# Kernel tuning notes

Measured on AMD Instinct MI355X. Metric: run time of the kernel, lower is better.

Reference implementation:

```python
import jax, jax.numpy as jnp
import numpy as np

N, E, NB = 50000, 100000, 6          # nodes, directed messages, max neighbors
NF, BF, H, DEPTH = 98, 6, 256, 6     # node feat, bond feat, hidden, depth
EF = NF + BF                          # edge_fdim: hmess = [fnode[src], bond_feats]


def setup_inputs() -> dict:
    key = jax.random.key(0)
    ks = jax.random.split(key, 12)
    s = lambda fan: np.float32(1.0 / np.sqrt(fan))
    return {
        "fnode": jax.random.normal(ks[0], (N, NF), jnp.float32),
        "fmess_idx": jax.random.randint(ks[1], (E, 2), 0, N),
        "fmess_feat": jax.random.normal(ks[2], (E, BF), jnp.float32),
        "agraph": jax.random.randint(ks[3], (N, NB), 0, E),
        "bgraph": jax.random.randint(ks[4], (E, NB), 0, E),
        "Wz": jax.random.normal(ks[5], (3, EF + H, H), jnp.float32) * s(EF + H),
        "bz": jnp.zeros((3, H), jnp.float32),
        "Wr": jax.random.normal(ks[6], (3, EF, H), jnp.float32) * s(EF),
        "Ur": jax.random.normal(ks[7], (3, H, H), jnp.float32) * s(H),
        "bur": jnp.zeros((3, H), jnp.float32),
        "Wh": jax.random.normal(ks[8], (3, EF + H, H), jnp.float32) * s(EF + H),
        "bh": jnp.zeros((3, H), jnp.float32),
        "Wo": jax.random.normal(ks[9], (3, NF + H, H), jnp.float32) * s(NF + H),
        "bo": jnp.zeros((3, H), jnp.float32),
    }


def _mpn(hnode, hmess, agraph, bgraph, Wz, bz, Wr, Ur, bur, Wh, bh, Wo, bo):
    # One MPNLayer: depth-unrolled message GRU over bgraph, then node readout via agraph.
    e_mask = jnp.ones((hmess.shape[0], 1), hmess.dtype).at[0, 0].set(0.0)  # msg 0 = padding
    r1 = hmess @ Wr  # W_r(fmess), loop-invariant  [E,H]

    def step(h, _):
        h_nei = h[bgraph]                                    # [E,NB,H] gather inbound msgs
        sum_h = h_nei.sum(axis=1)
        z = jax.nn.sigmoid(jnp.concatenate([hmess, sum_h], axis=1) @ Wz + bz)
        r = jax.nn.sigmoid(r1[:, None, :] + h_nei @ Ur + bur)  # [E,NB,H]
        sum_gh = (r * h_nei).sum(axis=1)
        pre_h = jnp.tanh(jnp.concatenate([hmess, sum_gh], axis=1) @ Wh + bh)
        return ((1.0 - z) * sum_h + z * pre_h) * e_mask, None

    h0 = jnp.zeros((hmess.shape[0], bz.shape[0]), hmess.dtype)
    h, _ = jax.lax.scan(step, h0, None, length=DEPTH)
    nei = h[agraph].sum(axis=1)                              # [N,H]
    node_h = jax.nn.relu(jnp.concatenate([hnode, nei], axis=1) @ Wo + bo)
    n_mask = jnp.ones((hnode.shape[0], 1), hnode.dtype).at[0, 0].set(0.0)  # node 0 = padding
    return node_h * n_mask


def reference(fnode, fmess_idx, fmess_feat, agraph, bgraph,
              Wz, bz, Wr, Ur, bur, Wh, bh, Wo, bo):
    # embed_graph: gather source-node features, concat with bond features
    hmess = jnp.concatenate([fnode[fmess_idx[:, 0]], fmess_feat], axis=1)  # [E,EF]
    run = jax.vmap(lambda a, b, c, d, e, f, g, hh, i: _mpn(
        fnode, hmess, agraph, bgraph, a, b, c, d, e, f, g, hh, i))
    qkv = run(Wz, bz, Wr, Ur, bur, Wh, bh, Wo, bo)           # [3,N,H]: Q/K/V encoders batched
    return (qkv[0], qkv[1], qkv[2])
```

## Files before the change

### kernel.cpp

```cpp
#include <hip/hip_runtime.h>


#define NE 100000
#define NEP 100032
#define NN 50000

typedef unsigned short u16;
typedef short short8 __attribute__((ext_vector_type(8)));
typedef float f32x4 __attribute__((ext_vector_type(4)));
typedef unsigned short u16x4 __attribute__((ext_vector_type(4)));

__device__ __forceinline__ float b2f(u16 u) {
  union { unsigned int i; float f; } v; v.i = ((unsigned int)u) << 16; return v.f;
}
__device__ __forceinline__ u16 f2b(float f) {
  union { float f; unsigned int i; } v; v.f = f;
  unsigned int b = v.i;
  b += 0x7FFFu + ((b >> 16) & 1u);
  return (u16)(b >> 16);
}
__device__ __forceinline__ unsigned cvtpk(float lo, float hi) {
  unsigned r;
  asm("v_cvt_pk_bf16_f32 %0, %1, %2" : "=v"(r) : "v"(lo), "v"(hi));
  return r;
}
__device__ __forceinline__ float sigm(float x) { return 1.0f / (1.0f + __expf(-x)); }
__device__ __forceinline__ float tanh_f(float x) { return 2.0f / (1.0f + __expf(-2.0f * x)) - 1.0f; }
__device__ __forceinline__ f32x4 mfma16(short8 a, short8 b, f32x4 c) {
  return __builtin_amdgcn_mfma_f32_16x16x32_bf16(a, b, c, 0, 0, 0);
}

__global__ void pack_wpre(const float* __restrict__ Wr, const float* __restrict__ Wz,
                          const float* __restrict__ Wh, u16* __restrict__ dst) {
  const int g = blockIdx.y;
  const int p = blockIdx.x * 256 + threadIdx.x;
  const int j = p & 7, l = (p >> 3) & 63, q = p >> 9;
  const int nb = q % 48, s = q / 48;
  const int k = 32 * s + 8 * (l >> 4) + j;
  const int n = 16 * nb + (l & 15);
  float v = 0.f;
  if (k < 104) {
    if (n < 256)      v = Wr[((size_t)g * 104 + k) * 256 + n];
    else if (n < 512) v = Wz[((size_t)g * 360 + k) * 256 + (n - 256)];
    else              v = Wh[((size_t)g * 360 + k) * 256 + (n - 512)];
  }
  dst[(size_t)g * 98304 + p] = f2b(v);
}

__global__ void pack_wgate(const float* __restrict__ Wz, const float* __restrict__ Wh,
                           u16* __restrict__ dst) {
  const int g = blockIdx.y;
  const int p = blockIdx.x * 256 + threadIdx.x;
  const int j = p & 7, l = (p >> 3) & 63, q = p >> 9;
  const int nb = q % 32, s = q / 32;
  const int k = 32 * s + 8 * (l >> 4) + j;
  const int n = 16 * nb + (l & 15);
  float v = (n < 256) ? Wz[((size_t)g * 360 + 104 + k) * 256 + n]
                      : Wh[((size_t)g * 360 + 104 + k) * 256 + (n - 256)];
  dst[(size_t)g * 131072 + p] = f2b(v);
}

__global__ void pack_ur(const float* __restrict__ Ur, u16* __restrict__ dst) {
  const int g = blockIdx.y;
  const int p = blockIdx.x * 256 + threadIdx.x;
  const int j = p & 7, l = (p >> 3) & 63, q = p >> 9;
  const int nb = q % 16, s = q / 16;
  const int k = 32 * s + 8 * (l >> 4) + j;
  const int n = 16 * nb + (l & 15);
  dst[(size_t)g * 65536 + p] = f2b(Ur[((size_t)g * 256 + k) * 256 + n]);
}

__global__ void pack_wo(const float* __restrict__ Wo, u16* __restrict__ dst) {
  const int g = blockIdx.y;
  const int p = blockIdx.x * 256 + threadIdx.x;
  const int j = p & 7, l = (p >> 3) & 63, q = p >> 9;
  const int nb = q % 16, s = q / 16;
  const int k = 32 * s + 8 * (l >> 4) + j;
  const int n = 16 * nb + (l & 15);
  float v = 0.f;
  if (k < 98)        v = Wo[((size_t)g * 354 + k) * 256 + n];
  else if (k >= 128) v = Wo[((size_t)g * 354 + (k - 30)) * 256 + n];
  dst[(size_t)g * 98304 + p] = f2b(v);
}

__global__ void embed_hmess_f(const float* __restrict__ fnode, const int* __restrict__ fmess_idx,
                              const float* __restrict__ fmess_feat, u16* __restrict__ hmF) {
  const int e = blockIdx.x * 2 + (threadIdx.x >> 7);
  const int c = threadIdx.x & 127;
  const int src = fmess_idx[e * 2];
  float v = 0.f;
  if (c < 98)       v = fnode[(size_t)src * 98 + c];
  else if (c < 104) v = fmess_feat[(size_t)e * 6 + (c - 98)];
  hmF[(size_t)(e >> 4) * 2048 + ((c >> 5) * 64 + (e & 15) + 16 * ((c >> 3) & 3)) * 8 + (c & 7)] = f2b(v);
}

__global__ void embed_fnode(const float* __restrict__ fnode, u16* __restrict__ fnp) {
  const int n = blockIdx.x * 2 + (threadIdx.x >> 7);
  const int c = threadIdx.x & 127;
  float v = (c < 98) ? fnode[(size_t)n * 98 + c] : 0.f;
  fnp[(size_t)n * 128 + c] = f2b(v);
}

__global__ __launch_bounds__(256)
void pre_gemm_t(const u16* __restrict__ hmF, const u16* __restrict__ Wpre,
                const float* __restrict__ bur, const float* __restrict__ bz,
                const float* __restrict__ bh, u16* __restrict__ r1b,
                u16* __restrict__ zpF, u16* __restrict__ hpF) {
  const int tid = threadIdx.x, wave = tid >> 6, lane = tid & 63;
  const int row0 = lane & 15, kq = lane >> 4;
  const int e0 = blockIdx.x * 32;
  const int cchunk = blockIdx.y;
  f32x4 acc[2][4];
#pragma unroll
  for (int i = 0; i < 2; ++i)
#pragma unroll
    for (int n = 0; n < 4; ++n) { acc[i][n][0]=0.f; acc[i][n][1]=0.f; acc[i][n][2]=0.f; acc[i][n][3]=0.f; }
#pragma unroll
  for (int kc = 0; kc < 4; ++kc) {
    short8 bf[2];
#pragma unroll
    for (int ef = 0; ef < 2; ++ef)
      bf[ef] = *(const short8*)(hmF + (size_t)((e0 >> 4) + ef) * 2048 + (size_t)(kc * 64 + lane) * 8);
#pragma unroll
    for (int nf = 0; nf < 4; ++nf) {
      const int nb = cchunk * 16 + wave * 4 + nf;
      short8 wf = *(const short8*)(Wpre + ((size_t)(kc * 48 + nb) * 64 + lane) * 8);
      acc[0][nf] = mfma16(wf, bf[0], acc[0][nf]);
      acc[1][nf] = mfma16(wf, bf[1], acc[1][nf]);
    }
  }
  const float* bias = (cchunk == 0) ? bur : (cchunk == 1 ? bz : bh);
  u16* dstF = (cchunk == 1) ? zpF : hpF;
#pragma unroll
  for (int ef = 0; ef < 2; ++ef)
#pragma unroll
    for (int nf = 0; nf < 4; ++nf) {
      const int n256 = wave * 64 + nf * 16 + kq * 4;
      const int e = e0 + ef * 16 + row0;
      u16x4 o;
#pragma unroll
      for (int v = 0; v < 4; ++v) o[v] = f2b(acc[ef][nf][v] + bias[n256 + v]);
      if (cchunk == 0) {
        *(u16x4*)(r1b + (size_t)e * 256 + n256) = o;
      } else {
        *(u16x4*)(dstF + ((size_t)((e0 >> 4) + ef) * 16 + (wave * 4 + nf)) * 256 + lane * 4) = o;
      }
    }
}

__global__ __launch_bounds__(512, 4)
void mpn_fused(const u16* __restrict__ HBin, u16* __restrict__ HBout,
               const u16* __restrict__ r1b, const int* __restrict__ bgraph,
               const u16* __restrict__ zpF, const u16* __restrict__ hpF,
               const u16* __restrict__ Wgate, const u16* __restrict__ Urp) {
  __shared__ __align__(16) u16 sF[16384];
  const int tid = threadIdx.x;
  const int wn = tid >> 6, lane = tid & 63;
  const int row0 = lane & 15, kq = lane >> 4;
  const int e0 = blockIdx.x * 32;

  {
    const int c0 = 4 * lane;
    const int offc = ((c0 >> 5) * 64 + 16 * ((c0 >> 3) & 3)) * 8 + (c0 & 7);
#pragma unroll 2
    for (int rr = 0; rr < 4; ++rr) {
      const int r = wn * 4 + rr;
      const int e = e0 + r;
      const u16x4 r1v = *(const u16x4*)(r1b + (size_t)e * 256 + c0);
      int idx[6];
#pragma unroll
      for (int k = 0; k < 6; ++k) idx[k] = bgraph[e * 6 + k];
      u16x4 hv[6], huv[6];
#pragma unroll
      for (int k = 0; k < 6; ++k) {
        const u16* rowp = HBin + (size_t)idx[k] * 512;
        hv[k]  = *(const u16x4*)(rowp + c0);
        huv[k] = *(const u16x4*)(rowp + 256 + c0);
      }
      float sh[4] = {0.f, 0.f, 0.f, 0.f}, sg[4] = {0.f, 0.f, 0.f, 0.f};
#pragma unroll
      for (int k = 0; k < 6; ++k)
#pragma unroll
        for (int j = 0; j < 4; ++j) {
          const float h  = b2f(hv[k][j]);
          const float rg = sigm(b2f(r1v[j]) + b2f(huv[k][j]));
          sh[j] += h;
          sg[j] += rg * h;
        }
      const int off = (r >> 4) * 4096 + offc + (r & 15) * 8;
      union { unsigned w[2]; u16x4 q; } p0, p1;
      p0.w[0] = cvtpk(sh[0], sh[1]); p0.w[1] = cvtpk(sh[2], sh[3]);
      p1.w[0] = cvtpk(sg[0], sg[1]); p1.w[1] = cvtpk(sg[2], sg[3]);
      *(u16x4*)(sF + off) = p0.q;
      *(u16x4*)(sF + 8192 + off) = p1.q;
    }
  }
  __syncthreads();

  f32x4 aZ[2][2], aH[2][2];
#pragma unroll
  for (int nf = 0; nf < 2; ++nf)
#pragma unroll
    for (int ef = 0; ef < 2; ++ef) {
      aZ[nf][ef][0]=0.f; aZ[nf][ef][1]=0.f; aZ[nf][ef][2]=0.f; aZ[nf][ef][3]=0.f;
      aH[nf][ef][0]=0.f; aH[nf][ef][1]=0.f; aH[nf][ef][2]=0.f; aH[nf][ef][3]=0.f;
    }
#pragma unroll
  for (int kc = 0; kc < 8; ++kc) {
    short8 wz0 = *(const short8*)(Wgate + ((size_t)(kc * 32 + wn * 2 + 0) * 64 + lane) * 8);
    short8 wz1 = *(const short8*)(Wgate + ((size_t)(kc * 32 + wn * 2 + 1) * 64 + lane) * 8);
    short8 wh0 = *(const short8*)(Wgate + ((size_t)(kc * 32 + 16 + wn * 2 + 0) * 64 + lane) * 8);
    short8 wh1 = *(const short8*)(Wgate + ((size_t)(kc * 32 + 16 + wn * 2 + 1) * 64 + lane) * 8);
#pragma unroll
    for (int ef = 0; ef < 2; ++ef) {
      short8 bsh = *(const short8*)(sF + ef * 4096 + (kc * 64 + lane) * 8);
      short8 bsg = *(const short8*)(sF + 8192 + ef * 4096 + (kc * 64 + lane) * 8);
      aZ[0][ef] = mfma16(wz0, bsh, aZ[0][ef]);
      aZ[1][ef] = mfma16(wz1, bsh, aZ[1][ef]);
      aH[0][ef] = mfma16(wh0, bsg, aH[0][ef]);
      aH[1][ef] = mfma16(wh1, bsg, aH[1][ef]);
    }
  }

  u16x4 hq[2][2];
#pragma unroll
  for (int nf = 0; nf < 2; ++nf) {
    const int lp = row0 + 16 * (nf * 2 + (kq >> 1));
    const int jo = 4 * (kq & 1);
    const int nc = wn * 2 + nf;
#pragma unroll
    for (int ef = 0; ef < 2; ++ef) {
      const int e = e0 + ef * 16 + row0;
      const int as = ef * 4096 + (wn * 64 + lp) * 8 + jo;
      const u16x4 shv = *(const u16x4*)(sF + as);
      const size_t tb = ((size_t)((e0 >> 4) + ef) * 16 + nc) * 256 + lane * 4;
      const u16x4 zp4 = *(const u16x4*)(zpF + tb);
      const u16x4 hp4 = *(const u16x4*)(hpF + tb);
      float hf[4];
#pragma unroll
      for (int v = 0; v < 4; ++v) {
        const float z  = sigm(b2f(zp4[v]) + aZ[nf][ef][v]);
        const float ph = tanh_f(b2f(hp4[v]) + aH[nf][ef][v]);
        float h = (1.0f - z) * b2f(shv[v]) + z * ph;
        if (e == 0) h = 0.f;
        hf[v] = h;
      }
      union { unsigned w[2]; u16x4 q; } pk;
      pk.w[0] = cvtpk(hf[0], hf[1]);
      pk.w[1] = cvtpk(hf[2], hf[3]);
      hq[nf][ef] = pk.q;
    }
  }
  __syncthreads();

#pragma unroll
  for (int nf = 0; nf < 2; ++nf) {
    const int lp = row0 + 16 * (nf * 2 + (kq >> 1));
    const int jo = 4 * (kq & 1);
#pragma unroll
    for (int ef = 0; ef < 2; ++ef)
      *(u16x4*)(sF + 8192 + ef * 4096 + (wn * 64 + lp) * 8 + jo) = hq[nf][ef];
  }
  __syncthreads();

  f32x4 aU[2][2];
#pragma unroll
  for (int nf = 0; nf < 2; ++nf)
#pragma unroll
    for (int ef = 0; ef < 2; ++ef) { aU[nf][ef][0]=0.f; aU[nf][ef][1]=0.f; aU[nf][ef][2]=0.f; aU[nf][ef][3]=0.f; }
#pragma unroll
  for (int kc = 0; kc < 8; ++kc) {
    short8 u0 = *(const short8*)(Urp + ((size_t)(kc * 16 + wn * 2 + 0) * 64 + lane) * 8);
    short8 u1 = *(const short8*)(Urp + ((size_t)(kc * 16 + wn * 2 + 1) * 64 + lane) * 8);
#pragma unroll
    for (int ef = 0; ef < 2; ++ef) {
      short8 hb = *(const short8*)(sF + 8192 + ef * 4096 + (kc * 64 + lane) * 8);
      aU[0][ef] = mfma16(u0, hb, aU[0][ef]);
      aU[1][ef] = mfma16(u1, hb, aU[1][ef]);
    }
  }

  {
    const int r = tid >> 4;
    const int e = e0 + r;
#pragma unroll
    for (int it = 0; it < 2; ++it) {
      const int c = (tid & 15) * 8 + it * 128;
      const short8 val = *(const short8*)(sF + 8192 + (r >> 4) * 4096 +
                         (((c >> 5) * 64 + (r & 15) + 16 * ((c >> 3) & 3)) * 8));
      *(short8*)(HBout + (size_t)e * 512 + c) = val;
    }
  }
#pragma unroll
  for (int nf = 0; nf < 2; ++nf) {
    const int lp = row0 + 16 * (nf * 2 + (kq >> 1));
    const int jo = 4 * (kq & 1);
#pragma unroll
    for (int ef = 0; ef < 2; ++ef) {
      union { unsigned w[2]; u16x4 q; } pk;
      pk.w[0] = cvtpk(aU[nf][ef][0], aU[nf][ef][1]);
      pk.w[1] = cvtpk(aU[nf][ef][2], aU[nf][ef][3]);
      *(u16x4*)(sF + ef * 4096 + (wn * 64 + lp) * 8 + jo) = pk.q;
    }
  }
  __syncthreads();

  {
    const int r = tid >> 4;
    const int e = e0 + r;
#pragma unroll
    for (int it = 0; it < 2; ++it) {
      const int c = (tid & 15) * 8 + it * 128;
      const short8 val = *(const short8*)(sF + (r >> 4) * 4096 +
                         (((c >> 5) * 64 + (r & 15) + 16 * ((c >> 3) & 3)) * 8));
      *(short8*)(HBout + (size_t)e * 512 + 256 + c) = val;
    }
  }
}

__global__ __launch_bounds__(512, 4)
void step0(u16* __restrict__ HB, const u16* __restrict__ zpF, const u16* __restrict__ hpF,
           const u16* __restrict__ Urp) {
  __shared__ __align__(16) u16 sHn[16384];
  const int tid = threadIdx.x;
  const int wn = tid >> 6, lane = tid & 63;
  const int row0 = lane & 15, kq = lane >> 4;
  const int e0 = blockIdx.x * 64;

#pragma unroll
  for (int nf = 0; nf < 2; ++nf) {
    const int lp = row0 + 16 * (nf * 2 + (kq >> 1));
    const int jo = 4 * (kq & 1);
    const int nc = wn * 2 + nf;
#pragma unroll
    for (int ef = 0; ef < 4; ++ef) {
      const int ev = (e0 + ef * 16) < NE;
      const int e  = e0 + ef * 16 + row0;
      const size_t tb = ((size_t)((e0 >> 4) + ef) * 16 + nc) * 256 + lane * 4;
      const u16x4 zp4 = *(const u16x4*)(zpF + tb);
      const u16x4 hp4 = *(const u16x4*)(hpF + tb);
      u16x4 hq;
#pragma unroll
      for (int v = 0; v < 4; ++v) {
        float hf = sigm(b2f(zp4[v])) * tanh_f(b2f(hp4[v]));
        if (e == 0 || !ev) hf = 0.f;
        hq[v] = f2b(hf);
      }
      *(u16x4*)(sHn + (size_t)ef * 4096 + (size_t)(wn * 64 + lp) * 8 + jo) = hq;
    }
  }
  __syncthreads();

  f32x4 aU[2][4];
#pragma unroll
  for (int nf = 0; nf < 2; ++nf)
#pragma unroll
    for (int ef = 0; ef < 4; ++ef) { aU[nf][ef][0]=0.f; aU[nf][ef][1]=0.f; aU[nf][ef][2]=0.f; aU[nf][ef][3]=0.f; }
#pragma unroll
  for (int kc = 0; kc < 8; ++kc) {
    short8 u0 = *(const short8*)(Urp + ((size_t)(kc * 16 + wn * 2 + 0) * 64 + lane) * 8);
    short8 u1 = *(const short8*)(Urp + ((size_t)(kc * 16 + wn * 2 + 1) * 64 + lane) * 8);
#pragma unroll
    for (int ef = 0; ef < 4; ++ef) {
      short8 hb = *(const short8*)(sHn + (size_t)ef * 4096 + (size_t)(kc * 64 + lane) * 8);
      aU[0][ef] = mfma16(u0, hb, aU[0][ef]);
      aU[1][ef] = mfma16(u1, hb, aU[1][ef]);
    }
  }
  {
    const int r = tid >> 3;
    const int e = e0 + r;
    if (e < NE) {
#pragma unroll
      for (int it = 0; it < 4; ++it) {
        const int c = (tid & 7) * 8 + it * 64;
        const short8 val = *(const short8*)(sHn + (size_t)(r >> 4) * 4096 +
                           (size_t)(((c >> 5) * 64 + (r & 15) + 16 * ((c >> 3) & 3)) * 8));
        *(short8*)(HB + (size_t)e * 512 + c) = val;
      }
    }
  }
  __syncthreads();
#pragma unroll
  for (int nf = 0; nf < 2; ++nf) {
    const int lp = row0 + 16 * (nf * 2 + (kq >> 1));
    const int jo = 4 * (kq & 1);
#pragma unroll
    for (int ef = 0; ef < 4; ++ef) {
      u16x4 uq;
#pragma unroll
      for (int v = 0; v < 4; ++v) uq[v] = f2b(aU[nf][ef][v]);
      *(u16x4*)(sHn + (size_t)ef * 4096 + (size_t)(wn * 64 + lp) * 8 + jo) = uq;
    }
  }
  __syncthreads();
  {
    const int r = tid >> 3;
    const int e = e0 + r;
    if (e < NE) {
#pragma unroll
      for (int it = 0; it < 4; ++it) {
        const int c = (tid & 7) * 8 + it * 64;
        const short8 val = *(const short8*)(sHn + (size_t)(r >> 4) * 4096 +
                           (size_t)(((c >> 5) * 64 + (r & 15) + 16 * ((c >> 3) & 3)) * 8));
        *(short8*)(HB + (size_t)e * 512 + 256 + c) = val;
      }
    }
  }
}

__global__ __launch_bounds__(256)
void readout(const u16* __restrict__ HB, const u16* __restrict__ fnp,
             const int* __restrict__ agraph, const u16* __restrict__ Wop,
             const float* __restrict__ bo, float* __restrict__ out) {
  __shared__ __align__(16) u16 sN[32][264];
  const int tid = threadIdx.x, wave = tid >> 6, lane = tid & 63;
  const int n0 = blockIdx.x * 32;
  const int row0 = lane & 15, kq = lane >> 4;

#pragma unroll 2
  for (int rr = 0; rr < 8; ++rr) {
    const int r = wave * 8 + rr;
    const int n = n0 + r;
    float s4[4] = {0.f, 0.f, 0.f, 0.f};
    if (n < NN) {
#pragma unroll
      for (int k = 0; k < 6; ++k) {
        const int idx = agraph[n * 6 + k];
        const u16x4 hv = *(const u16x4*)(HB + (size_t)idx * 512 + 4 * lane);
#pragma unroll
        for (int j = 0; j < 4; ++j) s4[j] += b2f(hv[j]);
      }
    }
#pragma unroll
    for (int j = 0; j < 4; ++j) sN[r][4 * lane + j] = f2b(s4[j]);
  }
  __syncthreads();

  f32x4 acc[2][4];
#pragma unroll
  for (int i = 0; i < 2; ++i)
#pragma unroll
    for (int n = 0; n < 4; ++n) { acc[i][n][0]=0.f; acc[i][n][1]=0.f; acc[i][n][2]=0.f; acc[i][n][3]=0.f; }
  const int ra = min(n0 + row0, NN - 1);
  const int rb = min(n0 + 16 + row0, NN - 1);
#pragma unroll
  for (int s = 0; s < 12; ++s) {
    short8 a0, a1;
    if (s < 4) {
      a0 = *(const short8*)(fnp + (size_t)ra * 128 + s * 32 + kq * 8);
      a1 = *(const short8*)(fnp + (size_t)rb * 128 + s * 32 + kq * 8);
    } else {
      a0 = *(const short8*)&sN[row0][(s - 4) * 32 + kq * 8];
      a1 = *(const short8*)&sN[row0 + 16][(s - 4) * 32 + kq * 8];
    }
#pragma unroll
    for (int ni = 0; ni < 4; ++ni) {
      short8 b = *(const short8*)(Wop + ((size_t)(s * 16 + wave * 4 + ni) * 64 + lane) * 8);
      acc[0][ni] = mfma16(a0, b, acc[0][ni]);
      acc[1][ni] = mfma16(a1, b, acc[1][ni]);
    }
  }
#pragma unroll
  for (int mi = 0; mi < 2; ++mi)
#pragma unroll
    for (int ni = 0; ni < 4; ++ni)
#pragma unroll
      for (int v = 0; v < 4; ++v) {
        const int m = mi * 16 + kq * 4 + v;
        const int col = wave * 64 + ni * 16 + row0;
        const int n = n0 + m;
        if (n < NN) {
          float val = fmaxf(acc[mi][ni][v] + bo[col], 0.f);
          if (n == 0) val = 0.f;
          out[(size_t)n * 256 + col] = val;
        }
      }
}

extern "C" void kernel_launch(void* const* d_in, const int* in_sizes, int n_in,
                              void* d_out, int out_size, void* d_ws, size_t ws_size,
                              hipStream_t stream) {
  const float* fnode      = (const float*)d_in[0];
  const int*   fmess_idx  = (const int*)d_in[1];
  const float* fmess_feat = (const float*)d_in[2];
  const int*   agraph     = (const int*)d_in[3];
  const int*   bgraph     = (const int*)d_in[4];
  const float* Wz         = (const float*)d_in[5];
  const float* bz         = (const float*)d_in[6];
  const float* Wr         = (const float*)d_in[7];
  const float* Ur         = (const float*)d_in[8];
  const float* bur        = (const float*)d_in[9];
  const float* Wh         = (const float*)d_in[10];
  const float* bh         = (const float*)d_in[11];
  const float* Wo         = (const float*)d_in[12];
  const float* bo         = (const float*)d_in[13];
  float* out = (float*)d_out;

  char* ws = (char*)d_ws;
  size_t off = 0;
  auto carve = [&](size_t bytes) -> char* {
    char* p = ws + off;
    off += (bytes + 511) & ~(size_t)511;
    return p;
  };
  u16* HB0  = (u16*)carve((size_t)NEP * 512 * 2);
  u16* HB1  = (u16*)carve((size_t)NEP * 512 * 2);
  u16* r1b  = (u16*)carve((size_t)NEP * 256 * 2);
  u16* zpF  = (u16*)carve((size_t)NEP * 256 * 2);
  u16* hpF  = (u16*)carve((size_t)NEP * 256 * 2);
  u16* hmF  = (u16*)carve((size_t)NEP * 128 * 2);
  u16* fnp  = (u16*)carve((size_t)NN * 128 * 2);
  u16* wpre = (u16*)carve((size_t)3 * 98304 * 2);
  u16* wgate= (u16*)carve((size_t)3 * 131072 * 2);
  u16* urp  = (u16*)carve((size_t)3 * 65536 * 2);
  u16* wop  = (u16*)carve((size_t)3 * 98304 * 2);
  if (off > ws_size) return;

  pack_wpre <<<dim3(384, 3), 256, 0, stream>>>(Wr, Wz, Wh, wpre);
  pack_wgate<<<dim3(512, 3), 256, 0, stream>>>(Wz, Wh, wgate);
  pack_ur   <<<dim3(256, 3), 256, 0, stream>>>(Ur, urp);
  pack_wo   <<<dim3(384, 3), 256, 0, stream>>>(Wo, wop);
  embed_hmess_f<<<NE / 2, 256, 0, stream>>>(fnode, fmess_idx, fmess_feat, hmF);
  embed_fnode<<<NN / 2, 256, 0, stream>>>(fnode, fnp);

  for (int g = 0; g < 3; ++g) {
    pre_gemm_t<<<dim3(NEP / 32, 3), 256, 0, stream>>>(
        hmF, wpre + (size_t)g * 98304, bur + g * 256, bz + g * 256, bh + g * 256,
        r1b, zpF, hpF);
    const u16* wgate_g = wgate + (size_t)g * 131072;
    const u16* urp_g   = urp + (size_t)g * 65536;
    step0<<<NEP / 64, 512, 0, stream>>>(HB0, zpF, hpF, urp_g);
    u16* bufs[2] = {HB0, HB1};
    int cur = 0;
    for (int d = 1; d < 6; ++d) {
      mpn_fused<<<NE / 32, 512, 0, stream>>>(bufs[cur], bufs[1 - cur], r1b, bgraph,
                                             zpF, hpF, wgate_g, urp_g);
      cur ^= 1;
    }
    readout<<<(NN + 31) / 32, 256, 0, stream>>>(
        bufs[cur], fnp, agraph, wop + (size_t)g * 98304, bo + g * 256, out + (size_t)g * NN * 256);
  }
}
```

Before: 3.493 ms.

## Fuse hmess pre-projection GEMM into step0 and mpn_fused, recomputing per depth

Drops the separate pre_gemm kernel that wrote r1, z-pre and h-pre activations to global memory. step0 and each mpn_fused launch now recompute the hmess projection (K=128) with MFMA in-kernel, keep the r1 tile in shared memory and add biases directly. This trades extra MFMA work per depth step, plus more shared memory and registers per block, for removing a launch and the global writes and reads of three E×256 bf16 tensors. step0 also moves from 64-row to 32-row blocks.

```diff
diff --git a/kernel.cpp b/kernel.cpp
--- a/kernel.cpp
+++ b/kernel.cpp
@@ -2,12 +2,12 @@
 
 
 #define NE 100000
-#define NEP 100032
 #define NN 50000
 
 typedef unsigned short u16;
 typedef short short8 __attribute__((ext_vector_type(8)));
 typedef float f32x4 __attribute__((ext_vector_type(4)));
+typedef float floatx4 __attribute__((ext_vector_type(4)));
 typedef unsigned short u16x4 __attribute__((ext_vector_type(4)));
 
 __device__ __forceinline__ float b2f(u16 u) {
@@ -101,63 +101,61 @@
   fnp[(size_t)n * 128 + c] = f2b(v);
 }
 
-__global__ __launch_bounds__(256)
-void pre_gemm_t(const u16* __restrict__ hmF, const u16* __restrict__ Wpre,
-                const float* __restrict__ bur, const float* __restrict__ bz,
-                const float* __restrict__ bh, u16* __restrict__ r1b,
-                u16* __restrict__ zpF, u16* __restrict__ hpF) {
-  const int tid = threadIdx.x, wave = tid >> 6, lane = tid & 63;
-  const int row0 = lane & 15, kq = lane >> 4;
-  const int e0 = blockIdx.x * 32;
-  const int cchunk = blockIdx.y;
-  f32x4 acc[2][4];
-#pragma unroll
-  for (int i = 0; i < 2; ++i)
-#pragma unroll
-    for (int n = 0; n < 4; ++n) { acc[i][n][0]=0.f; acc[i][n][1]=0.f; acc[i][n][2]=0.f; acc[i][n][3]=0.f; }
-#pragma unroll
-  for (int kc = 0; kc < 4; ++kc) {
-    short8 bf[2];
-#pragma unroll
-    for (int ef = 0; ef < 2; ++ef)
-      bf[ef] = *(const short8*)(hmF + (size_t)((e0 >> 4) + ef) * 2048 + (size_t)(kc * 64 + lane) * 8);
-#pragma unroll
-    for (int nf = 0; nf < 4; ++nf) {
-      const int nb = cchunk * 16 + wave * 4 + nf;
-      short8 wf = *(const short8*)(Wpre + ((size_t)(kc * 48 + nb) * 64 + lane) * 8);
-      acc[0][nf] = mfma16(wf, bf[0], acc[0][nf]);
-      acc[1][nf] = mfma16(wf, bf[1], acc[1][nf]);
-    }
-  }
-  const float* bias = (cchunk == 0) ? bur : (cchunk == 1 ? bz : bh);
-  u16* dstF = (cchunk == 1) ? zpF : hpF;
-#pragma unroll
-  for (int ef = 0; ef < 2; ++ef)
-#pragma unroll
-    for (int nf = 0; nf < 4; ++nf) {
-      const int n256 = wave * 64 + nf * 16 + kq * 4;
-      const int e = e0 + ef * 16 + row0;
-      u16x4 o;
-#pragma unroll
-      for (int v = 0; v < 4; ++v) o[v] = f2b(acc[ef][nf][v] + bias[n256 + v]);
-      if (cchunk == 0) {
-        *(u16x4*)(r1b + (size_t)e * 256 + n256) = o;
-      } else {
-        *(u16x4*)(dstF + ((size_t)((e0 >> 4) + ef) * 16 + (wave * 4 + nf)) * 256 + lane * 4) = o;
-      }
-    }
-}
-
 __global__ __launch_bounds__(512, 4)
 void mpn_fused(const u16* __restrict__ HBin, u16* __restrict__ HBout,
-               const u16* __restrict__ r1b, const int* __restrict__ bgraph,
-               const u16* __restrict__ zpF, const u16* __restrict__ hpF,
-               const u16* __restrict__ Wgate, const u16* __restrict__ Urp) {
+               const u16* __restrict__ hmF, const int* __restrict__ bgraph,
+               const u16* __restrict__ Wpre, const u16* __restrict__ Wgate,
+               const u16* __restrict__ Urp, const float* __restrict__ bur,
+               const float* __restrict__ bz, const float* __restrict__ bh) {
   __shared__ __align__(16) u16 sF[16384];
+  __shared__ __align__(16) u16 sR1[8448];
   const int tid = threadIdx.x;
   const int wn = tid >> 6, lane = tid & 63;
   const int row0 = lane & 15, kq = lane >> 4;
   const int e0 = blockIdx.x * 32;
+
+  f32x4 aZ[2][2], aH[2][2], aR[2][2];
+#pragma unroll
+  for (int nf = 0; nf < 2; ++nf)
+#pragma unroll
+    for (int ef = 0; ef < 2; ++ef) {
+      aZ[nf][ef][0]=0.f; aZ[nf][ef][1]=0.f; aZ[nf][ef][2]=0.f; aZ[nf][ef][3]=0.f;
+      aH[nf][ef][0]=0.f; aH[nf][ef][1]=0.f; aH[nf][ef][2]=0.f; aH[nf][ef][3]=0.f;
+      aR[nf][ef][0]=0.f; aR[nf][ef][1]=0.f; aR[nf][ef][2]=0.f; aR[nf][ef][3]=0.f;
+    }
+#pragma unroll
+  for (int kc = 0; kc < 4; ++kc) {
+    short8 bm[2];
+#pragma unroll
+    for (int ef = 0; ef < 2; ++ef)
+      bm[ef] = *(const short8*)(hmF + (size_t)((e0 >> 4) + ef) * 2048 + (size_t)(kc * 64 + lane) * 8);
+#pragma unroll
+    for (int nf = 0; nf < 2; ++nf) {
+      const int nb = wn * 2 + nf;
+      short8 wr = *(const short8*)(Wpre + ((size_t)(kc * 48 + nb) * 64 + lane) * 8);
+      short8 wz = *(const short8*)(Wpre + ((size_t)(kc * 48 + 16 + nb) * 64 + lane) * 8);
+      short8 wh = *(const short8*)(Wpre + ((size_t)(kc * 48 + 32 + nb) * 64 + lane) * 8);
+#pragma unroll
+      for (int ef = 0; ef < 2; ++ef) {
+        aR[nf][ef] = mfma16(wr, bm[ef], aR[nf][ef]);
+        aZ[nf][ef] = mfma16(wz, bm[ef], aZ[nf][ef]);
+        aH[nf][ef] = mfma16(wh, bm[ef], aH[nf][ef]);
+      }
+    }
+  }
+#pragma unroll
+  for (int nf = 0; nf < 2; ++nf) {
+    const int n = wn * 32 + nf * 16 + kq * 4;
+    const floatx4 bv = *(const floatx4*)(bur + n);
+#pragma unroll
+    for (int ef = 0; ef < 2; ++ef) {
+      union { unsigned w[2]; u16x4 q; } pk;
+      pk.w[0] = cvtpk(aR[nf][ef][0] + bv[0], aR[nf][ef][1] + bv[1]);
+      pk.w[1] = cvtpk(aR[nf][ef][2] + bv[2], aR[nf][ef][3] + bv[3]);
+      *(u16x4*)(sR1 + (ef * 16 + row0) * 264 + n) = pk.q;
+    }
+  }
+  __syncthreads();
 
   {
     const int c0 = 4 * lane;
@@ -166,7 +164,7 @@
     for (int rr = 0; rr < 4; ++rr) {
       const int r = wn * 4 + rr;
       const int e = e0 + r;
-      const u16x4 r1v = *(const u16x4*)(r1b + (size_t)e * 256 + c0);
+      const u16x4 r1v = *(const u16x4*)(sR1 + r * 264 + c0);
       int idx[6];
 #pragma unroll
       for (int k = 0; k < 6; ++k) idx[k] = bgraph[e * 6 + k];
@@ -197,14 +195,6 @@
   }
   __syncthreads();
 
-  f32x4 aZ[2][2], aH[2][2];
-#pragma unroll
-  for (int nf = 0; nf < 2; ++nf)
-#pragma unroll
-    for (int ef = 0; ef < 2; ++ef) {
-      aZ[nf][ef][0]=0.f; aZ[nf][ef][1]=0.f; aZ[nf][ef][2]=0.f; aZ[nf][ef][3]=0.f;
-      aH[nf][ef][0]=0.f; aH[nf][ef][1]=0.f; aH[nf][ef][2]=0.f; aH[nf][ef][3]=0.f;
-    }
 #pragma unroll
   for (int kc = 0; kc < 8; ++kc) {
     short8 wz0 = *(const short8*)(Wgate + ((size_t)(kc * 32 + wn * 2 + 0) * 64 + lane) * 8);
@@ -227,20 +217,19 @@
   for (int nf = 0; nf < 2; ++nf) {
     const int lp = row0 + 16 * (nf * 2 + (kq >> 1));
     const int jo = 4 * (kq & 1);
-    const int nc = wn * 2 + nf;
+    const int n = wn * 32 + nf * 16 + kq * 4;
+    const floatx4 bzv = *(const floatx4*)(bz + n);
+    const floatx4 bhv = *(const floatx4*)(bh + n);
 #pragma unroll
     for (int ef = 0; ef < 2; ++ef) {
       const int e = e0 + ef * 16 + row0;
       const int as = ef * 4096 + (wn * 64 + lp) * 8 + jo;
       const u16x4 shv = *(const u16x4*)(sF + as);
-      const size_t tb = ((size_t)((e0 >> 4) + ef) * 16 + nc) * 256 + lane * 4;
-      const u16x4 zp4 = *(const u16x4*)(zpF + tb);
-      const u16x4 hp4 = *(const u16x4*)(hpF + tb);
       float hf[4];
 #pragma unroll
       for (int v = 0; v < 4; ++v) {
-        const float z  = sigm(b2f(zp4[v]) + aZ[nf][ef][v]);
-        const float ph = tanh_f(b2f(hp4[v]) + aH[nf][ef][v]);
+        const float z  = sigm(aZ[nf][ef][v] + bzv[v]);
+        const float ph = tanh_f(aH[nf][ef][v] + bhv[v]);
         float h = (1.0f - z) * b2f(shv[v]) + z * ph;
         if (e == 0) h = 0.f;
         hf[v] = h;
@@ -319,65 +308,92 @@
 }
 
 __global__ __launch_bounds__(512, 4)
-void step0(u16* __restrict__ HB, const u16* __restrict__ zpF, const u16* __restrict__ hpF,
-           const u16* __restrict__ Urp) {
-  __shared__ __align__(16) u16 sHn[16384];
+void step0(u16* __restrict__ HB, const u16* __restrict__ hmF,
+           const u16* __restrict__ Wpre, const u16* __restrict__ Urp,
+           const float* __restrict__ bz, const float* __restrict__ bh) {
+  __shared__ __align__(16) u16 sHn[8192];
   const int tid = threadIdx.x;
   const int wn = tid >> 6, lane = tid & 63;
   const int row0 = lane & 15, kq = lane >> 4;
-  const int e0 = blockIdx.x * 64;
+  const int e0 = blockIdx.x * 32;
+
+  f32x4 aZ[2][2], aH[2][2];
+#pragma unroll
+  for (int nf = 0; nf < 2; ++nf)
+#pragma unroll
+    for (int ef = 0; ef < 2; ++ef) {
+      aZ[nf][ef][0]=0.f; aZ[nf][ef][1]=0.f; aZ[nf][ef][2]=0.f; aZ[nf][ef][3]=0.f;
+      aH[nf][ef][0]=0.f; aH[nf][ef][1]=0.f; aH[nf][ef][2]=0.f; aH[nf][ef][3]=0.f;
+    }
+#pragma unroll
+  for (int kc = 0; kc < 4; ++kc) {
+    short8 bm[2];
+#pragma unroll
+    for (int ef = 0; ef < 2; ++ef)
+      bm[ef] = *(const short8*)(hmF + (size_t)((e0 >> 4) + ef) * 2048 + (size_t)(kc * 64 + lane) * 8);
+#pragma unroll
+    for (int nf = 0; nf < 2; ++nf) {
+      const int nb = wn * 2 + nf;
+      short8 wz = *(const short8*)(Wpre + ((size_t)(kc * 48 + 16 + nb) * 64 + lane) * 8);
+      short8 wh = *(const short8*)(Wpre + ((size_t)(kc * 48 + 32 + nb) * 64 + lane) * 8);
+#pragma unroll
+      for (int ef = 0; ef < 2; ++ef) {
+        aZ[nf][ef] = mfma16(wz, bm[ef], aZ[nf][ef]);
+        aH[nf][ef] = mfma16(wh, bm[ef], aH[nf][ef]);
+      }
+    }
+  }
 
 #pragma unroll
   for (int nf = 0; nf < 2; ++nf) {
     const int lp = row0 + 16 * (nf * 2 + (kq >> 1));
     const int jo = 4 * (kq & 1);
-    const int nc = wn * 2 + nf;
-#pragma unroll
-    for (int ef = 0; ef < 4; ++ef) {
-      const int ev = (e0 + ef * 16) < NE;
-      const int e  = e0 + ef * 16 + row0;
-      const size_t tb = ((size_t)((e0 >> 4) + ef) * 16 + nc) * 256 + lane * 4;
-      const u16x4 zp4 = *(const u16x4*)(zpF + tb);
-      const u16x4 hp4 = *(const u16x4*)(hpF + tb);
-      u16x4 hq;
+    const int n = wn * 32 + nf * 16 + kq * 4;
+    const floatx4 bzv = *(const floatx4*)(bz + n);
+    const floatx4 bhv = *(const floatx4*)(bh + n);
+#pragma unroll
+    for (int ef = 0; ef < 2; ++ef) {
+      const int e = e0 + ef * 16 + row0;
+      float hf[4];
 #pragma unroll
       for (int v = 0; v < 4; ++v) {
-        float hf = sigm(b2f(zp4[v])) * tanh_f(b2f(hp4[v]));
-        if (e == 0 || !ev) hf = 0.f;
-        hq[v] = f2b(hf);
-      }
-      *(u16x4*)(sHn + (size_t)ef * 4096 + (size_t)(wn * 64 + lp) * 8 + jo) = hq;
-    }
-  }
-  __syncthreads();
-
-  f32x4 aU[2][4];
+        float h = sigm(aZ[nf][ef][v] + bzv[v]) * tanh_f(aH[nf][ef][v] + bhv[v]);
+        if (e == 0) h = 0.f;
+        hf[v] = h;
+      }
+      union { unsigned w[2]; u16x4 q; } pk;
+      pk.w[0] = cvtpk(hf[0], hf[1]);
+      pk.w[1] = cvtpk(hf[2], hf[3]);
+      *(u16x4*)(sHn + ef * 4096 + (wn * 64 + lp) * 8 + jo) = pk.q;
+    }
+  }
+  __syncthreads();
+
+  f32x4 aU[2][2];
 #pragma unroll
   for (int nf = 0; nf < 2; ++nf)
 #pragma unroll
-    for (int ef = 0; ef < 4; ++ef) { aU[nf][ef][0]=0.f; aU[nf][ef][1]=0.f; aU[nf][ef][2]=0.f; aU[nf][ef][3]=0.f; }
+    for (int ef = 0; ef < 2; ++ef) { aU[nf][ef][0]=0.f; aU[nf][ef][1]=0.f; aU[nf][ef][2]=0.f; aU[nf][ef][3]=0.f; }
 #pragma unroll
   for (int kc = 0; kc < 8; ++kc) {
     short8 u0 = *(const short8*)(Urp + ((size_t)(kc * 16 + wn * 2 + 0) * 64 + lane) * 8);
     short8 u1 = *(const short8*)(Urp + ((size_t)(kc * 16 + wn * 2 + 1) * 64 + lane) * 8);
 #pragma unroll
-    for (int ef = 0; ef < 4; ++ef) {
-      short8 hb = *(const short8*)(sHn + (size_t)ef * 4096 + (size_t)(kc * 64 + lane) * 8);
+    for (int ef = 0; ef < 2; ++ef) {
+      short8 hb = *(const short8*)(sHn + ef * 4096 + (kc * 64 + lane) * 8);
       aU[0][ef] = mfma16(u0, hb, aU[0][ef]);
       aU[1][ef] = mfma16(u1, hb, aU[1][ef]);
     }
   }
   {
-    const int r = tid >> 3;
+    const int r = tid >> 4;
     const int e = e0 + r;
-    if (e < NE) {
-#pragma unroll
-      for (int it = 0; it < 4; ++it) {
-        const int c = (tid & 7) * 8 + it * 64;
-        const short8 val = *(const short8*)(sHn + (size_t)(r >> 4) * 4096 +
-                           (size_t)(((c >> 5) * 64 + (r & 15) + 16 * ((c >> 3) & 3)) * 8));
-        *(short8*)(HB + (size_t)e * 512 + c) = val;
-      }
+#pragma unroll
+    for (int it = 0; it < 2; ++it) {
+      const int c = (tid & 15) * 8 + it * 128;
+      const short8 val = *(const short8*)(sHn + (r >> 4) * 4096 +
+                         (((c >> 5) * 64 + (r & 15) + 16 * ((c >> 3) & 3)) * 8));
+      *(short8*)(HB + (size_t)e * 512 + c) = val;
     }
   }
   __syncthreads();
@@ -386,25 +402,23 @@
     const int lp = row0 + 16 * (nf * 2 + (kq >> 1));
     const int jo = 4 * (kq & 1);
 #pragma unroll
-    for (int ef = 0; ef < 4; ++ef) {
-      u16x4 uq;
-#pragma unroll
-      for (int v = 0; v < 4; ++v) uq[v] = f2b(aU[nf][ef][v]);
-      *(u16x4*)(sHn + (size_t)ef * 4096 + (size_t)(wn * 64 + lp) * 8 + jo) = uq;
+    for (int ef = 0; ef < 2; ++ef) {
+      union { unsigned w[2]; u16x4 q; } pk;
+      pk.w[0] = cvtpk(aU[nf][ef][0], aU[nf][ef][1]);
+      pk.w[1] = cvtpk(aU[nf][ef][2], aU[nf][ef][3]);
+      *(u16x4*)(sHn + ef * 4096 + (wn * 64 + lp) * 8 + jo) = pk.q;
     }
   }
   __syncthreads();
   {
-    const int r = tid >> 3;
+    const int r = tid >> 4;
     const int e = e0 + r;
-    if (e < NE) {
-#pragma unroll
-      for (int it = 0; it < 4; ++it) {
-        const int c = (tid & 7) * 8 + it * 64;
-        const short8 val = *(const short8*)(sHn + (size_t)(r >> 4) * 4096 +
-                           (size_t)(((c >> 5) * 64 + (r & 15) + 16 * ((c >> 3) & 3)) * 8));
-        *(short8*)(HB + (size_t)e * 512 + 256 + c) = val;
-      }
+#pragma unroll
+    for (int it = 0; it < 2; ++it) {
+      const int c = (tid & 15) * 8 + it * 128;
+      const short8 val = *(const short8*)(sHn + (r >> 4) * 4096 +
+                         (((c >> 5) * 64 + (r & 15) + 16 * ((c >> 3) & 3)) * 8));
+      *(short8*)(HB + (size_t)e * 512 + 256 + c) = val;
     }
   }
 }
@@ -504,12 +518,9 @@
     off += (bytes + 511) & ~(size_t)511;
     return p;
   };
-  u16* HB0  = (u16*)carve((size_t)NEP * 512 * 2);
-  u16* HB1  = (u16*)carve((size_t)NEP * 512 * 2);
-  u16* r1b  = (u16*)carve((size_t)NEP * 256 * 2);
-  u16* zpF  = (u16*)carve((size_t)NEP * 256 * 2);
-  u16* hpF  = (u16*)carve((size_t)NEP * 256 * 2);
-  u16* hmF  = (u16*)carve((size_t)NEP * 128 * 2);
+  u16* HB0  = (u16*)carve((size_t)NE * 512 * 2);
+  u16* HB1  = (u16*)carve((size_t)NE * 512 * 2);
+  u16* hmF  = (u16*)carve((size_t)NE * 128 * 2);
   u16* fnp  = (u16*)carve((size_t)NN * 128 * 2);
   u16* wpre = (u16*)carve((size_t)3 * 98304 * 2);
   u16* wgate= (u16*)carve((size_t)3 * 131072 * 2);
@@ -525,17 +536,18 @@
   embed_fnode<<<NN / 2, 256, 0, stream>>>(fnode, fnp);
 
   for (int g = 0; g < 3; ++g) {
-    pre_gemm_t<<<dim3(NEP / 32, 3), 256, 0, stream>>>(
-        hmF, wpre + (size_t)g * 98304, bur + g * 256, bz + g * 256, bh + g * 256,
-        r1b, zpF, hpF);
+    const u16* wpre_g  = wpre + (size_t)g * 98304;
     const u16* wgate_g = wgate + (size_t)g * 131072;
     const u16* urp_g   = urp + (size_t)g * 65536;
-    step0<<<NEP / 64, 512, 0, stream>>>(HB0, zpF, hpF, urp_g);
+    const float* bur_g = bur + g * 256;
+    const float* bz_g  = bz + g * 256;
+    const float* bh_g  = bh + g * 256;
+    step0<<<NE / 32, 512, 0, stream>>>(HB0, hmF, wpre_g, urp_g, bz_g, bh_g);
     u16* bufs[2] = {HB0, HB1};
     int cur = 0;
     for (int d = 1; d < 6; ++d) {
-      mpn_fused<<<NE / 32, 512, 0, stream>>>(bufs[cur], bufs[1 - cur], r1b, bgraph,
-                                             zpF, hpF, wgate_g, urp_g);
+      mpn_fused<<<NE / 32, 512, 0, stream>>>(bufs[cur], bufs[1 - cur], hmF, bgraph,
+                                             wpre_g, wgate_g, urp_g, bur_g, bz_g, bh_g);
       cur ^= 1;
     }
     readout<<<(NN + 31) / 32, 256, 0, stream>>>(
```

After: 3.439 ms. No clear change (-1.6%).
